# Optimization experiments

Measured on AMD Instinct MI355X. Metric: run time of the kernel, lower is better.

The kernel has to match this reference:

```python
import jax, jax.numpy as jnp
import numpy as np

B, N, C, M, OUT = 4, 256, 32, 4, 64


def _uniform(k, shape, fan_in):
    s = 1.0 / np.sqrt(fan_in)
    return jax.random.uniform(k, shape, jnp.float32, -s, s)


def setup_inputs() -> dict:
    key = jax.random.key(0)
    ks = jax.random.split(key, 11)
    return {
        "x": jax.random.normal(ks[0], (B, N, N, C), jnp.float32),
        # Neighborhood / SnConv2to1 linears (in=C, out=M neighborhood channels)
        "w1_nb": _uniform(ks[1], (3 * C, M), 3 * C),
        "b1_nb": _uniform(ks[2], (M,), 3 * C),
        "w0_nb": _uniform(ks[3], (2 * C, M), 2 * C),
        "b0_nb": _uniform(ks[4], (M,), 2 * C),
        # SnConv2 linears (in channels = M*C after neighborhood product)
        "w2d": _uniform(ks[5], (2 * M * C, OUT), 2 * M * C),
        "b2d": _uniform(ks[6], (OUT,), 2 * M * C),
        "w1d": _uniform(ks[7], (3 * M * C, OUT), 3 * M * C),
        "b1d": _uniform(ks[8], (OUT,), 3 * M * C),
        "w0d": _uniform(ks[9], (2 * M * C, OUT), 2 * M * C),
        "b0d": _uniform(ks[10], (OUT,), 2 * M * C),
    }


def _contractions(x):
    # x: [B, n, n, c]; mask=None, reduction='mean' path of _get_contractions
    n = x.shape[1]
    rowsum = x.sum(axis=1) / n                      # [B, n, c]
    colsum = x.sum(axis=2) / n                      # [B, n, c]
    diag = jnp.diagonal(x, axis1=1, axis2=2)        # [B, c, n]
    rowcolsum = x.sum(axis=(1, 2)) / (n * n)        # [B, c]
    diag_sum = diag.sum(axis=-1) / n                # [B, c]  (/= sqrt(n^2))
    diag = jnp.moveaxis(diag, -1, 1)                # move_from_end -> [B, n, c]
    return rowsum, colsum, diag, rowcolsum, diag_sum


def reference(x, w1_nb, b1_nb, w0_nb, b0_nb, w2d, b2d, w1d, b1d, w0d, b0d):
    # ---- Neighborhood: SnConv2to1 -> sigmoid ----
    rs, cs, dg, rcs, ds = _contractions(x)
    obj1 = jnp.concatenate([rs, cs, dg], axis=-1)             # [B, n, 3C]
    obj0 = jnp.concatenate([rcs, ds], axis=-1)                # [B, 2C]
    node = obj1 @ w1_nb + b1_nb + (obj0 @ w0_nb + b0_nb)[:, None, :]
    neighbs = jax.nn.sigmoid(node)                            # [B, n, M]
    # ---- _neighbor_elementwise_product ----
    expanded = neighbs[:, None, :, :] * neighbs[:, :, None, :]  # [B, n, n, M]
    # channel_product: outer product over channel dims, collapsed to M*C
    xl = (expanded[..., :, None] * x[..., None, :]).reshape(B, N, N, M * C)
    # ---- SnConv2 on the localized tensor ----
    rs2, cs2, dg2, rcs2, ds2 = _contractions(xl)
    obj2d = jnp.concatenate([xl, jnp.swapaxes(xl, 1, 2)], axis=-1)  # [B,n,n,2MC]
    obj1d = jnp.concatenate([rs2, cs2, dg2], axis=-1)               # [B,n,3MC]
    obj0d = jnp.concatenate([rcs2, ds2], axis=-1)                   # [B,2MC]
    out = (obj2d @ w2d + b2d
           + (obj1d @ w1d + b1d)[:, None, :, :]
           + (obj0d @ w0d + b0d)[:, None, None, :])                 # [B,n,n,OUT]
    return out
```

## Files before the change

kernel.cpp:

```cpp
#include <hip/hip_runtime.h>
#include <math.h>

#define Bv 4
#define Nv 256
#define Cv 32
#define Mv 4
#define OUTv 64
#define MCv (Mv*Cv)

typedef _Float16 h8 __attribute__((ext_vector_type(8)));
typedef _Float16 h4 __attribute__((ext_vector_type(4)));
typedef float f4 __attribute__((ext_vector_type(4)));

__device__ __align__(16) float g_rs  [Bv * Nv * Cv];
__device__ __align__(16) float g_cs  [Bv * Nv * Cv];
__device__ __align__(16) float g_dgx [Bv * Nv * Cv];
__device__ __align__(16) float g_nb  [Bv * Nv * Mv];
__device__ __align__(16) float g_S1  [Bv * Nv * MCv];
__device__ __align__(16) float g_S2  [Bv * Nv * MCv];
__device__ __align__(16) float g_rcs2[Bv * MCv];
__device__ __align__(16) float g_ds2 [Bv * MCv];
__device__ __align__(16) float g_t0g [Bv * OUTv];
__device__ __align__(16) float g_addv[Bv * Nv * OUTv];
__device__ __align__(16) _Float16 g_wfrag[8 * 4 * 64 * 8];

__global__ void k_wpackz(const float* __restrict__ w2d) {
    int t = threadIdx.x;
    int r = blockIdx.x;
    if (r == 8) {
        if (t < 128) ((float4*)g_rcs2)[t] = {0.f,0.f,0.f,0.f};
        else         ((float4*)g_ds2)[t - 128] = {0.f,0.f,0.f,0.f};
        return;
    }
    int fi = r * 256 + t;
    int s = fi >> 8, q = (fi >> 6) & 3, lane = fi & 63;
    int k0 = s * 32 + ((lane >> 4) << 3);
    int o = q * 16 + (lane & 15);
    #pragma unroll
    for (int jj = 0; jj < 8; jj++)
        g_wfrag[fi * 8 + jj] = (_Float16)w2d[(size_t)(k0 + jj) * OUTv + o];
}

__global__ __launch_bounds__(256) void k_contract1(const float* __restrict__ x) {
    int bx = blockIdx.x, b = blockIdx.y;
    int t = threadIdx.x, c4 = t & 7, sub = t >> 3;
    const float4* xb4 = (const float4*)(x + (size_t)b * Nv * Nv * Cv);
    __shared__ float red[32][36];
    float4 acc = {0.f,0.f,0.f,0.f};
    if (bx < Nv) {
        int n = bx;
        for (int i = sub; i < Nv; i += 32) {
            float4 v = xb4[((size_t)i * Nv + n) * 8 + c4];
            acc.x += v.x; acc.y += v.y; acc.z += v.z; acc.w += v.w;
        }
        red[sub][c4*4+0] = acc.x; red[sub][c4*4+1] = acc.y;
        red[sub][c4*4+2] = acc.z; red[sub][c4*4+3] = acc.w;
        __syncthreads();
        if (t < 32) {
            float s = 0.f;
            #pragma unroll
            for (int k = 0; k < 32; k++) s += red[k][t];
            g_rs[(b * Nv + n) * Cv + t] = s * (1.0f / Nv);
        }
        if (t < 8) ((float4*)g_dgx)[(b * Nv + n) * 8 + t] = xb4[((size_t)n * Nv + n) * 8 + t];
    } else {
        int n = bx - Nv;
        for (int j = sub; j < Nv; j += 32) {
            float4 v = xb4[((size_t)n * Nv + j) * 8 + c4];
            acc.x += v.x; acc.y += v.y; acc.z += v.z; acc.w += v.w;
        }
        red[sub][c4*4+0] = acc.x; red[sub][c4*4+1] = acc.y;
        red[sub][c4*4+2] = acc.z; red[sub][c4*4+3] = acc.w;
        __syncthreads();
        if (t < 32) {
            float s = 0.f;
            #pragma unroll
            for (int k = 0; k < 32; k++) s += red[k][t];
            g_cs[(b * Nv + n) * Cv + t] = s * (1.0f / Nv);
        }
    }
}

__global__ void k_neighb(const float* __restrict__ w1, const float* __restrict__ b1,
                         const float* __restrict__ w0, const float* __restrict__ b0) {
    int b = blockIdx.x, t = threadIdx.x;
    int c = t & 31, sub = t >> 5;
    float ar = 0.f, ad = 0.f;
    for (int n = sub; n < Nv; n += 8) {
        ar += g_rs[(b * Nv + n) * Cv + c];
        ad += g_dgx[(b * Nv + n) * Cv + c];
    }
    __shared__ float red[8][64];
    __shared__ float obj0[64];
    __shared__ float t0nb[4];
    red[sub][c] = ar;
    red[sub][32 + c] = ad;
    __syncthreads();
    if (t < 64) {
        float s = 0.f;
        #pragma unroll
        for (int k = 0; k < 8; k++) s += red[k][t];
        obj0[t] = s * (1.0f / Nv);
    }
    __syncthreads();
    if (t < 4) {
        float v = b0[t];
        for (int k = 0; k < 2 * Cv; k++) v += obj0[k] * w0[k * Mv + t];
        t0nb[t] = v;
    }
    __syncthreads();
    int n = t;
    float node[4];
    #pragma unroll
    for (int m = 0; m < 4; m++) node[m] = t0nb[m] + b1[m];
    for (int cc = 0; cc < Cv; cc++) {
        float r = g_rs[(b * Nv + n) * Cv + cc];
        float s = g_cs[(b * Nv + n) * Cv + cc];
        float d = g_dgx[(b * Nv + n) * Cv + cc];
        #pragma unroll
        for (int m = 0; m < 4; m++)
            node[m] += r * w1[cc * Mv + m] + s * w1[(Cv + cc) * Mv + m] + d * w1[(2 * Cv + cc) * Mv + m];
    }
    #pragma unroll
    for (int m = 0; m < 4; m++)
        g_nb[(b * Nv + n) * Mv + m] = 1.0f / (1.0f + expf(-node[m]));
}

__global__ __launch_bounds__(256) void k_wsum(const float* __restrict__ x) {
    int bx = blockIdx.x, b = blockIdx.y;
    int t = threadIdx.x, c4 = t & 7, sub = t >> 3;
    __shared__ __align__(16) float4 nbl[Nv];
    if (t < Nv) nbl[t] = ((const float4*)(g_nb + (size_t)b * Nv * Mv))[t];
    __syncthreads();
    const float4* xb4 = (const float4*)(x + (size_t)b * Nv * Nv * Cv);
    float4 a[4];
    #pragma unroll
    for (int m = 0; m < 4; m++) a[m] = {0.f,0.f,0.f,0.f};
    __shared__ float red[32][132];
    if (bx < Nv) {
        int n = bx;
        for (int i = sub; i < Nv; i += 32) {
            float4 v = xb4[((size_t)i * Nv + n) * 8 + c4];
            float4 nv = nbl[i];
            a[0].x += nv.x*v.x; a[0].y += nv.x*v.y; a[0].z += nv.x*v.z; a[0].w += nv.x*v.w;
            a[1].x += nv.y*v.x; a[1].y += nv.y*v.y; a[1].z += nv.y*v.z; a[1].w += nv.y*v.w;
            a[2].x += nv.z*v.x; a[2].y += nv.z*v.y; a[2].z += nv.z*v.z; a[2].w += nv.z*v.w;
            a[3].x += nv.w*v.x; a[3].y += nv.w*v.y; a[3].z += nv.w*v.z; a[3].w += nv.w*v.w;
        }
        #pragma unroll
        for (int m = 0; m < 4; m++) {
            red[sub][m*32 + c4*4+0] = a[m].x; red[sub][m*32 + c4*4+1] = a[m].y;
            red[sub][m*32 + c4*4+2] = a[m].z; red[sub][m*32 + c4*4+3] = a[m].w;
        }
        __syncthreads();
        if (t < 128) {
            float s = 0.f;
            #pragma unroll
            for (int k = 0; k < 32; k++) s += red[k][t];
            g_S1[(size_t)(b * Nv + n) * MCv + t] = s;
            int m = t >> 5, c = t & 31;
            float nv = ((const float*)&nbl[n])[m];
            atomicAdd(&g_rcs2[b * MCv + t], nv * s);
            atomicAdd(&g_ds2 [b * MCv + t], nv * nv * g_dgx[(b * Nv + n) * Cv + c]);
        }
    } else {
        int n = bx - Nv;
        for (int j = sub; j < Nv; j += 32) {
            float4 v = xb4[((size_t)n * Nv + j) * 8 + c4];
            float4 nv = nbl[j];
            a[0].x += nv.x*v.x; a[0].y += nv.x*v.y; a[0].z += nv.x*v.z; a[0].w += nv.x*v.w;
            a[1].x += nv.y*v.x; a[1].y += nv.y*v.y; a[1].z += nv.y*v.z; a[1].w += nv.y*v.w;
            a[2].x += nv.z*v.x; a[2].y += nv.z*v.y; a[2].z += nv.z*v.z; a[2].w += nv.z*v.w;
            a[3].x += nv.w*v.x; a[3].y += nv.w*v.y; a[3].z += nv.w*v.z; a[3].w += nv.w*v.w;
        }
        #pragma unroll
        for (int m = 0; m < 4; m++) {
            red[sub][m*32 + c4*4+0] = a[m].x; red[sub][m*32 + c4*4+1] = a[m].y;
            red[sub][m*32 + c4*4+2] = a[m].z; red[sub][m*32 + c4*4+3] = a[m].w;
        }
        __syncthreads();
        if (t < 128) {
            float s = 0.f;
            #pragma unroll
            for (int k = 0; k < 32; k++) s += red[k][t];
            g_S2[(size_t)(b * Nv + n) * MCv + t] = s;
        }
    }
}

__global__ void k_t0(const float* __restrict__ w0d, const float* __restrict__ b0d) {
    int b = blockIdx.x, t = threadIdx.x;
    __shared__ float rc[MCv], ds[MCv];
    rc[t] = g_rcs2[b * MCv + t] * (1.0f / ((float)Nv * Nv));
    ds[t] = g_ds2 [b * MCv + t] * (1.0f / Nv);
    __syncthreads();
    if (t < OUTv) {
        float v = b0d[t];
        for (int k = 0; k < MCv; k++)
            v += rc[k] * w0d[k * OUTv + t] + ds[k] * w0d[(MCv + k) * OUTv + t];
        g_t0g[b * OUTv + t] = v;
    }
}

__global__ __launch_bounds__(256) void k_add(const float* __restrict__ w1d,
                                             const float* __restrict__ b1d,
                                             const float* __restrict__ b2d) {
    int b = blockIdx.y, n = blockIdx.x;
    int t = threadIdx.x, o = t & 63, ks = t >> 6;
    __shared__ float red[4][64];
    const float invN = 1.0f / Nv;
    float nv = g_nb[(b * Nv + n) * Mv + ks];
    float f = nv * invN, d2 = nv * nv;
    const float* S1r = g_S1 + (size_t)(b * Nv + n) * MCv + ks * 32;
    const float* S2r = g_S2 + (size_t)(b * Nv + n) * MCv + ks * 32;
    const float* dgr = g_dgx + (size_t)(b * Nv + n) * Cv;
    float acc = 0.f;
    #pragma unroll 8
    for (int c = 0; c < 32; c++) {
        int mc = ks * 32 + c;
        acc += f * S1r[c] * w1d[(size_t)mc * OUTv + o]
             + f * S2r[c] * w1d[(size_t)(MCv + mc) * OUTv + o]
             + d2 * dgr[c] * w1d[(size_t)(2 * MCv + mc) * OUTv + o];
    }
    red[ks][o] = acc;
    __syncthreads();
    if (t < 64) {
        float v = red[0][t] + red[1][t] + red[2][t] + red[3][t]
                + b1d[t] + b2d[t] + g_t0g[b * OUTv + t];
        g_addv[(size_t)(b * Nv + n) * OUTv + t] = v;
    }
}

#define XPAD 40
__global__ __launch_bounds__(256) void k_main(const float* __restrict__ x,
                                              float* __restrict__ out) {
    int jt = blockIdx.x, i = blockIdx.y, b = blockIdx.z;
    int j0 = jt * 128;
    int t = threadIdx.x;
    int lane = t & 63, w = t >> 6;
    int rowA = lane & 15, quad = lane >> 4;

    __shared__ __align__(16) _Float16 Wl[8 * 4 * 64 * 8];
    __shared__ __align__(16) _Float16 Xt[128 * XPAD];
    __shared__ __align__(16) _Float16 Xb[128 * XPAD];

    {
        const float4* src = (const float4*)g_wfrag;
        float4* dst = (float4*)Wl;
        #pragma unroll
        for (int r = 0; r < 8; r++) dst[r * 256 + t] = src[r * 256 + t];
    }
    {
        const float4* x4 = (const float4*)x;
        #pragma unroll
        for (int r = 0; r < 4; r++) {
            int idx = r * 256 + t;
            int j = idx >> 3, c4 = idx & 7;
            float4 v = x4[((size_t)(b * Nv + i) * Nv + j0 + j) * 8 + c4];
            h4 hv; hv[0] = (_Float16)v.x; hv[1] = (_Float16)v.y;
            hv[2] = (_Float16)v.z; hv[3] = (_Float16)v.w;
            *(h4*)&Xt[j * XPAD + c4 * 4] = hv;
            float4 u = x4[((size_t)(b * Nv + j0 + j) * Nv + i) * 8 + c4];
            h4 hu; hu[0] = (_Float16)u.x; hu[1] = (_Float16)u.y;
            hu[2] = (_Float16)u.z; hu[3] = (_Float16)u.w;
            *(h4*)&Xb[j * XPAD + c4 * 4] = hu;
        }
    }
    int jl1 = w * 32 + rowA, jl2 = jl1 + 16;
    _Float16 e1h[4], e2h[4];
    {
        const float* ni = g_nb + (size_t)(b * Nv + i) * Mv;
        const float* n1 = g_nb + (size_t)(b * Nv + j0 + jl1) * Mv;
        const float* n2 = g_nb + (size_t)(b * Nv + j0 + jl2) * Mv;
        #pragma unroll
        for (int m = 0; m < 4; m++) {
            e1h[m] = (_Float16)(ni[m] * n1[m]);
            e2h[m] = (_Float16)(ni[m] * n2[m]);
        }
    }
    __syncthreads();

    f4 acc[2][4];
    #pragma unroll
    for (int js = 0; js < 2; js++)
        #pragma unroll
        for (int q = 0; q < 4; q++) acc[js][q] = {0.f, 0.f, 0.f, 0.f};

    const h8* Wf = (const h8*)Wl;
    #pragma unroll
    for (int part = 0; part < 2; part++) {
        const _Float16* X = part ? Xb : Xt;
        h8 xv1 = *(const h8*)&X[jl1 * XPAD + quad * 8];
        h8 xv2 = *(const h8*)&X[jl2 * XPAD + quad * 8];
        #pragma unroll
        for (int m = 0; m < 4; m++) {
            h8 a1 = xv1 * e1h[m];
            h8 a2 = xv2 * e2h[m];
            int s = part * 4 + m;
            #pragma unroll
            for (int q = 0; q < 4; q++) {
                h8 bf = Wf[(s * 4 + q) * 64 + lane];
                acc[0][q] = __builtin_amdgcn_mfma_f32_16x16x32_f16(a1, bf, acc[0][q], 0, 0, 0);
                acc[1][q] = __builtin_amdgcn_mfma_f32_16x16x32_f16(a2, bf, acc[1][q], 0, 0, 0);
            }
        }
    }
    #pragma unroll
    for (int js = 0; js < 2; js++) {
        int jbase = j0 + w * 32 + js * 16 + quad * 4;
        #pragma unroll
        for (int q = 0; q < 4; q++) {
            int o = q * 16 + rowA;
            #pragma unroll
            for (int r = 0; r < 4; r++) {
                int j = jbase + r;
                float v = acc[js][q][r] + g_addv[(size_t)(b * Nv + j) * OUTv + o];
                out[(((size_t)(b * Nv + i)) * Nv + j) * OUTv + o] = v;
            }
        }
    }
}

extern "C" void kernel_launch(void* const* d_in, const int* in_sizes, int n_in,
                              void* d_out, int out_size, void* d_ws, size_t ws_size,
                              hipStream_t stream) {
    const float* x     = (const float*)d_in[0];
    const float* w1_nb = (const float*)d_in[1];
    const float* b1_nb = (const float*)d_in[2];
    const float* w0_nb = (const float*)d_in[3];
    const float* b0_nb = (const float*)d_in[4];
    const float* w2d   = (const float*)d_in[5];
    const float* b2d   = (const float*)d_in[6];
    const float* w1d   = (const float*)d_in[7];
    const float* b1d   = (const float*)d_in[8];
    const float* w0d   = (const float*)d_in[9];
    const float* b0d   = (const float*)d_in[10];
    float* out = (float*)d_out;
    (void)d_ws; (void)ws_size;

    hipLaunchKernelGGL(k_wpackz, dim3(9), dim3(256), 0, stream, w2d);
    hipLaunchKernelGGL(k_contract1, dim3(2 * Nv, Bv), dim3(256), 0, stream, x);
    hipLaunchKernelGGL(k_neighb, dim3(Bv), dim3(256), 0, stream,
                       w1_nb, b1_nb, w0_nb, b0_nb);
    hipLaunchKernelGGL(k_wsum, dim3(2 * Nv, Bv), dim3(256), 0, stream, x);
    hipLaunchKernelGGL(k_t0, dim3(Bv), dim3(128), 0, stream, w0d, b0d);
    hipLaunchKernelGGL(k_add, dim3(Nv, Bv), dim3(256), 0, stream,
                       w1d, b1d, b2d);
    hipLaunchKernelGGL(k_main, dim3(2, Nv, Bv), dim3(256), 0, stream, x, out);
}
```

Measured before the change: 183.4 us.

## Fold weight packing and t0 into other kernels, read W fragments from global

Merges the weight-fragment packing and accumulator zeroing into extra blocks of the first contraction kernel. It also folds the per-batch obj0 linear into the k_add reduction, which removes two small launches. k_main no longer stages the 32KB fp16 weight fragments into LDS; its MFMA B operands are read straight from global memory, relying on cache. In exchange, k_add recomputes the t0 term redundantly per row, and k_main issues global loads inside the MFMA loop.

```diff
diff --git a/kernel.cpp b/kernel.cpp
--- a/kernel.cpp
+++ b/kernel.cpp
@@ -20,30 +20,31 @@
 __device__ __align__(16) float g_S2  [Bv * Nv * MCv];
 __device__ __align__(16) float g_rcs2[Bv * MCv];
 __device__ __align__(16) float g_ds2 [Bv * MCv];
-__device__ __align__(16) float g_t0g [Bv * OUTv];
 __device__ __align__(16) float g_addv[Bv * Nv * OUTv];
 __device__ __align__(16) _Float16 g_wfrag[8 * 4 * 64 * 8];
 
-__global__ void k_wpackz(const float* __restrict__ w2d) {
+__global__ __launch_bounds__(256) void k_contract1(const float* __restrict__ x,
+                                                   const float* __restrict__ w2d) {
+    int bx = blockIdx.x, b = blockIdx.y;
     int t = threadIdx.x;
-    int r = blockIdx.x;
-    if (r == 8) {
-        if (t < 128) ((float4*)g_rcs2)[t] = {0.f,0.f,0.f,0.f};
-        else         ((float4*)g_ds2)[t - 128] = {0.f,0.f,0.f,0.f};
+    if (bx >= 2 * Nv) {
+        if (b != 0) return;
+        int r = bx - 2 * Nv;
+        if (r == 8) {
+            if (t < 128) ((float4*)g_rcs2)[t] = {0.f,0.f,0.f,0.f};
+            else         ((float4*)g_ds2)[t - 128] = {0.f,0.f,0.f,0.f};
+            return;
+        }
+        int fi = r * 256 + t;
+        int s = fi >> 8, q = (fi >> 6) & 3, lane = fi & 63;
+        int k0 = s * 32 + ((lane >> 4) << 3);
+        int o = q * 16 + (lane & 15);
+        #pragma unroll
+        for (int jj = 0; jj < 8; jj++)
+            g_wfrag[fi * 8 + jj] = (_Float16)w2d[(size_t)(k0 + jj) * OUTv + o];
         return;
     }
-    int fi = r * 256 + t;
-    int s = fi >> 8, q = (fi >> 6) & 3, lane = fi & 63;
-    int k0 = s * 32 + ((lane >> 4) << 3);
-    int o = q * 16 + (lane & 15);
-    #pragma unroll
-    for (int jj = 0; jj < 8; jj++)
-        g_wfrag[fi * 8 + jj] = (_Float16)w2d[(size_t)(k0 + jj) * OUTv + o];
-}
-
-__global__ __launch_bounds__(256) void k_contract1(const float* __restrict__ x) {
-    int bx = blockIdx.x, b = blockIdx.y;
-    int t = threadIdx.x, c4 = t & 7, sub = t >> 3;
+    int c4 = t & 7, sub = t >> 3;
     const float4* xb4 = (const float4*)(x + (size_t)b * Nv * Nv * Cv);
     __shared__ float red[32][36];
     float4 acc = {0.f,0.f,0.f,0.f};
@@ -188,45 +189,38 @@
     }
 }
 
-__global__ void k_t0(const float* __restrict__ w0d, const float* __restrict__ b0d) {
-    int b = blockIdx.x, t = threadIdx.x;
-    __shared__ float rc[MCv], ds[MCv];
-    rc[t] = g_rcs2[b * MCv + t] * (1.0f / ((float)Nv * Nv));
-    ds[t] = g_ds2 [b * MCv + t] * (1.0f / Nv);
-    __syncthreads();
-    if (t < OUTv) {
-        float v = b0d[t];
-        for (int k = 0; k < MCv; k++)
-            v += rc[k] * w0d[k * OUTv + t] + ds[k] * w0d[(MCv + k) * OUTv + t];
-        g_t0g[b * OUTv + t] = v;
-    }
-}
-
 __global__ __launch_bounds__(256) void k_add(const float* __restrict__ w1d,
                                              const float* __restrict__ b1d,
-                                             const float* __restrict__ b2d) {
+                                             const float* __restrict__ b2d,
+                                             const float* __restrict__ w0d,
+                                             const float* __restrict__ b0d) {
     int b = blockIdx.y, n = blockIdx.x;
     int t = threadIdx.x, o = t & 63, ks = t >> 6;
     __shared__ float red[4][64];
     const float invN = 1.0f / Nv;
+    const float invN2 = invN * invN;
     float nv = g_nb[(b * Nv + n) * Mv + ks];
     float f = nv * invN, d2 = nv * nv;
     const float* S1r = g_S1 + (size_t)(b * Nv + n) * MCv + ks * 32;
     const float* S2r = g_S2 + (size_t)(b * Nv + n) * MCv + ks * 32;
     const float* dgr = g_dgx + (size_t)(b * Nv + n) * Cv;
+    const float* rcr = g_rcs2 + b * MCv + ks * 32;
+    const float* dsr = g_ds2  + b * MCv + ks * 32;
     float acc = 0.f;
     #pragma unroll 8
     for (int c = 0; c < 32; c++) {
         int mc = ks * 32 + c;
         acc += f * S1r[c] * w1d[(size_t)mc * OUTv + o]
              + f * S2r[c] * w1d[(size_t)(MCv + mc) * OUTv + o]
-             + d2 * dgr[c] * w1d[(size_t)(2 * MCv + mc) * OUTv + o];
+             + d2 * dgr[c] * w1d[(size_t)(2 * MCv + mc) * OUTv + o]
+             + invN2 * rcr[c] * w0d[(size_t)mc * OUTv + o]
+             + invN  * dsr[c] * w0d[(size_t)(MCv + mc) * OUTv + o];
     }
     red[ks][o] = acc;
     __syncthreads();
     if (t < 64) {
         float v = red[0][t] + red[1][t] + red[2][t] + red[3][t]
-                + b1d[t] + b2d[t] + g_t0g[b * OUTv + t];
+                + b1d[t] + b2d[t] + b0d[t];
         g_addv[(size_t)(b * Nv + n) * OUTv + t] = v;
     }
 }
@@ -240,16 +234,9 @@
     int lane = t & 63, w = t >> 6;
     int rowA = lane & 15, quad = lane >> 4;
 
-    __shared__ __align__(16) _Float16 Wl[8 * 4 * 64 * 8];
     __shared__ __align__(16) _Float16 Xt[128 * XPAD];
     __shared__ __align__(16) _Float16 Xb[128 * XPAD];
 
-    {
-        const float4* src = (const float4*)g_wfrag;
-        float4* dst = (float4*)Wl;
-        #pragma unroll
-        for (int r = 0; r < 8; r++) dst[r * 256 + t] = src[r * 256 + t];
-    }
     {
         const float4* x4 = (const float4*)x;
         #pragma unroll
@@ -286,7 +273,7 @@
         #pragma unroll
         for (int q = 0; q < 4; q++) acc[js][q] = {0.f, 0.f, 0.f, 0.f};
 
-    const h8* Wf = (const h8*)Wl;
+    const h8* Wf = (const h8*)g_wfrag;
     #pragma unroll
     for (int part = 0; part < 2; part++) {
         const _Float16* X = part ? Xb : Xt;
@@ -338,13 +325,11 @@
     float* out = (float*)d_out;
     (void)d_ws; (void)ws_size;
 
-    hipLaunchKernelGGL(k_wpackz, dim3(9), dim3(256), 0, stream, w2d);
-    hipLaunchKernelGGL(k_contract1, dim3(2 * Nv, Bv), dim3(256), 0, stream, x);
+    hipLaunchKernelGGL(k_contract1, dim3(2 * Nv + 9, Bv), dim3(256), 0, stream, x, w2d);
     hipLaunchKernelGGL(k_neighb, dim3(Bv), dim3(256), 0, stream,
                        w1_nb, b1_nb, w0_nb, b0_nb);
     hipLaunchKernelGGL(k_wsum, dim3(2 * Nv, Bv), dim3(256), 0, stream, x);
-    hipLaunchKernelGGL(k_t0, dim3(Bv), dim3(128), 0, stream, w0d, b0d);
     hipLaunchKernelGGL(k_add, dim3(Nv, Bv), dim3(256), 0, stream,
-                       w1d, b1d, b2d);
+                       w1d, b1d, b2d, w0d, b0d);
     hipLaunchKernelGGL(k_main, dim3(2, Nv, Bv), dim3(256), 0, stream, x, out);
 }
```

After: 190.9 us. +4.1%, slower.
